# Kernel optimization log

Measured on AMD Instinct MI355X. Metric: run time of the kernel, lower is better.

The kernel has to match this reference:

```python
import jax, jax.numpy as jnp
import numpy as np
from jax import lax

B, C, H, W = 64, 64, 56, 56
E, TOPK = 8, 2
DN = ('NCHW', 'OIHW', 'NCHW')


def setup_inputs() -> dict:
    key = jax.random.key(0)
    ks = jax.random.split(key, 9)
    s = 0.05
    return {
        'x': jax.random.normal(ks[0], (B, C, H, W), jnp.float32),
        'gate_w': jax.random.normal(ks[1], (E, C), jnp.float32) * s,
        'gate_b': jnp.zeros((E,), jnp.float32),
        'conv1_w': jax.random.normal(ks[2], (E, C, C, 3, 3), jnp.float32) * s,
        'bn1_s': jnp.ones((E, C), jnp.float32),
        'bn1_b': jnp.zeros((E, C), jnp.float32),
        'conv2_w': jax.random.normal(ks[3], (E, C, C, 3, 3), jnp.float32) * s,
        'bn2_s': jnp.ones((E, C), jnp.float32),
        'bn2_b': jnp.zeros((E, C), jnp.float32),
    }


def _conv3x3(x, w):
    return lax.conv_general_dilated(x, w, (1, 1), ((1, 1), (1, 1)), dimension_numbers=DN)


def _bn(y, scale, bias):
    # eval-mode BatchNorm with running_mean=0, running_var=1 -> per-channel affine
    return y * scale[None, :, None, None] + bias[None, :, None, None]


def _basic_block(x, w1, s1, b1, w2, s2, b2):
    # standard ResNet BasicBlock, stride=1, identity downsample
    out = jax.nn.relu(_bn(_conv3x3(x, w1), s1, b1))
    out = _bn(_conv3x3(out, w2), s2, b2)
    return jax.nn.relu(out + x)


def reference(x, gate_w, gate_b, conv1_w, bn1_s, bn1_b, conv2_w, bn2_s, bn2_b):
    # gate: global average pool over HW -> linear -> top-k softmax weights [B, E]
    pooled = jnp.mean(x, axis=(2, 3))                       # [B, C]
    logits = pooled @ gate_w.T + gate_b                      # [B, E]
    top_vals, top_idx = lax.top_k(logits, TOPK)              # [B, K]
    top_w = jax.nn.softmax(top_vals, axis=-1)                # [B, K]
    dense_w = jnp.zeros((x.shape[0], E), x.dtype).at[
        jnp.arange(x.shape[0])[:, None], top_idx].set(top_w)  # [B, E]

    # run all experts (dense reference for the sparse dispatch/combine)
    ex_out = jax.vmap(lambda w1, s1, b1, w2, s2, b2: _basic_block(x, w1, s1, b1, w2, s2, b2))(
        conv1_w, bn1_s, bn1_b, conv2_w, bn2_s, bn2_b)        # [E, B, C, H, W]
    out = jnp.einsum('be,ebchw->bchw', dense_w, ex_out)
    return out, dense_w
```

## Files before the change

### kernel.cpp

```cpp
#include <hip/hip_runtime.h>


#define BATCH 64
#define CH    64
#define HW_   3136
#define IMG_  (CH*HW_)
#define PLANE (HW_*16)
#define NE    8
#define JOBS  128
#define PWSZ  36864
#define NTILE 13
#define BD    6
#define CGRID (NTILE*2*BATCH)

typedef unsigned short u16;
typedef __attribute__((ext_vector_type(8))) short short8_t;
typedef __attribute__((ext_vector_type(16))) float floatx16;

__device__ u16   g_xb[(size_t)BATCH*IMG_ + 4*PLANE];
__device__ u16   g_h[(size_t)JOBS*IMG_ + 4*PLANE];
__device__ u16   g_pw1[NE * PWSZ];
__device__ u16   g_pw2[NE * PWSZ];
__device__ int   g_eid[JOBS];
__device__ float g_wgt[JOBS];
__device__ float g_pool[49 * BATCH * CH];

__device__ __forceinline__ u16 f2b(float f) {
    unsigned v; __builtin_memcpy(&v, &f, 4);
    return (u16)((v + 0x7FFFu + ((v >> 16) & 1u)) >> 16);
}

__global__ __launch_bounds__(256) void prep_kernel(
    const float* __restrict__ x,
    const float* __restrict__ w1, const float* __restrict__ s1,
    const float* __restrict__ w2, const float* __restrict__ s2)
{
    int bid = blockIdx.x;
    int tid = threadIdx.x;
    if (bid < 2304) {
        int idx = bid * 256 + tid;
        int conv = idx / 294912;
        int i2 = idx - conv * 294912;
        int e = i2 / PWSZ;   int r = i2 - e * PWSZ;
        int s36 = r >> 10;   int r2 = r & 1023;
        int mt  = r2 >> 9;   int r3 = r2 & 511;
        int h   = r3 >> 8;   int r4 = r3 & 255;
        int m   = r4 >> 3;   int j  = r4 & 7;
        int tap = s36 >> 2;
        int ci  = ((s36 & 3) << 4) | (h << 3) | j;
        int M   = mt*32 + m;
        const float* w  = conv ? w2 : w1;
        const float* sc = conv ? s2 : s1;
        float v = w[((e*64 + M)*64 + ci)*9 + tap] * sc[e*64 + M];
        (conv ? g_pw2 : g_pw1)[i2] = f2b(v);
        return;
    }
    __shared__ u16 T[64*66];
    int xid = bid - 2304;
    int b = xid / 49;
    int tile = xid - b*49;
    int pos0 = tile * 64;
    int pin = tid & 63;
    int c0 = tid >> 6;
    const float* xb = x + (size_t)b*IMG_ + pos0 + pin;
    #pragma unroll
    for (int i = 0; i < 16; i++) {
        int ch = c0*16 + i;
        T[pin*66 + ch] = f2b(xb[ch*HW_]);
    }
    __syncthreads();
    u16* ob = g_xb + (size_t)b*IMG_ + (size_t)pos0*16;
    #pragma unroll
    for (int i = 0; i < 16; i++) {
        int j = tid + i*256;
        int kq  = j >> 10;
        int pos = (j >> 4) & 63;
        int c16 = j & 15;
        ob[(size_t)kq*PLANE + pos*16 + c16] = T[pos*66 + kq*16 + c16];
    }
    if (tid < 64) {
        float s = 0.f;
        const float* xc = x + (size_t)b*IMG_ + tid*HW_ + pos0;
        #pragma unroll 4
        for (int p = 0; p < 64; p++) s += xc[p];
        g_pool[tile*(BATCH*CH) + b*64 + tid] = s;
    }
}

__global__ __launch_bounds__(64) void gate_fin_kernel(
    const float* __restrict__ gw, const float* __restrict__ gb,
    float* __restrict__ dw_out)
{
    __shared__ float pooled[CH];
    __shared__ float logits[NE];
    int b = blockIdx.x, t = threadIdx.x;
    float s = 0.f;
    #pragma unroll
    for (int i = 0; i < 49; i++) s += g_pool[i*(BATCH*CH) + b*64 + t];
    pooled[t] = s * (1.f/3136.f);
    __syncthreads();
    if (t < NE) {
        float l = gb[t];
        for (int c = 0; c < CH; c++) l += pooled[c] * gw[t*CH + c];
        logits[t] = l;
    }
    __syncthreads();
    if (t == 0) {
        int i1 = 0; float v1 = logits[0];
        for (int e = 1; e < NE; e++) if (logits[e] > v1) { v1 = logits[e]; i1 = e; }
        int i2 = -1; float v2 = -3.4e38f;
        for (int e = 0; e < NE; e++) if (e != i1 && logits[e] > v2) { v2 = logits[e]; i2 = e; }
        float eb = __expf(v2 - v1);
        float wa = 1.f / (1.f + eb), wb = eb / (1.f + eb);
        for (int e = 0; e < NE; e++) dw_out[b*NE + e] = 0.f;
        dw_out[b*NE + i1] = wa;
        dw_out[b*NE + i2] = wb;
        g_eid[2*b] = i1; g_eid[2*b+1] = i2;
        g_wgt[2*b] = wa; g_wgt[2*b+1] = wb;
    }
}

__device__ __forceinline__ void stageA(
    u16* AL, const u16* __restrict__ pw0, const u16* __restrict__ pw1,
    int mt, int tid)
{
    short8_t st[9];
    #pragma unroll
    for (int i = 0; i < 9; i++) {
        int u = i*512 + tid;
        int es = u >= 2304;
        int r = u - (es ? 2304 : 0);
        int s36 = r >> 6;
        int c = r & 63;
        st[i] = *(const short8_t*)((es ? pw1 : pw0) + s36*1024 + mt*512 + c*8);
    }
    #pragma unroll
    for (int i = 0; i < 9; i++) {
        int u = i*512 + tid;
        int es = u >= 2304;
        int r = u - (es ? 2304 : 0);
        int s36 = r >> 6;
        int c = r & 63;
        *(short8_t*)(AL + (s36*2 + es)*512 + c*8) = st[i];
    }
}

__device__ __forceinline__ void mkOffs(
    unsigned* off, int gn, int y, int xc, int h, unsigned zoff)
{
    #pragma unroll
    for (int tap = 0; tap < 9; tap++) {
        int dy = tap/3 - 1, dx = tap - (tap/3)*3 - 1;
        int p = gn + dy*56 + dx;
        bool vld = ((unsigned)(y + dy) < 56u) && ((unsigned)(xc + dx) < 56u);
        off[tap] = vld ? (unsigned)(p*32 + h*16) : zoff;
    }
}
#define LOADB(bk, off) (*(const short8_t*)((bk) + (off)))

#define STEP_SGB(HAS_VMEM, HAS_DS)                                   \
    do {                                                             \
        if (HAS_VMEM) __builtin_amdgcn_sched_group_barrier(0x020, 2, 0); \
        if (HAS_DS)   __builtin_amdgcn_sched_group_barrier(0x100, 1, 0); \
        __builtin_amdgcn_sched_group_barrier(0x008, 2, 0);           \
    } while (0)

__global__ __launch_bounds__(512, 4) void conv1_kernel(const float* __restrict__ b1)
{
    __shared__ u16 AL[36864];
    int wg = blockIdx.x;
    int L  = (wg & 7) * (CGRID/8) + (wg >> 3);
    int b  = L / 26;
    int r  = L - b*26;
    int tile = r >> 1;
    int mt   = r & 1;
    int e0 = g_eid[2*b], e1 = g_eid[2*b+1];
    int tid = threadIdx.x;
    int lane = tid & 63, w = tid >> 6;
    int es = w & 1, pg = w >> 1;
    int l31 = lane & 31, h = lane >> 5;
    int gn0 = tile*256 + pg*64 + l31;
    int gn1 = gn0 + 32;
    int y0 = gn0/56, xc0 = gn0 - y0*56;
    int y1 = gn1/56, xc1 = gn1 - y1*56;
    int e = es ? e1 : e0;
    const char* base = (const char*)(g_xb + (size_t)b*IMG_);
    const char* bk0 = base;
    const char* bk1 = base + PLANE*2;
    const char* bk2 = base + 2*PLANE*2;
    const char* bk3 = base + 3*PLANE*2;
    unsigned zoff = (unsigned)((size_t)(BATCH - b)*IMG_*2);
    const u16* pw0 = g_pw1 + e0*PWSZ;
    const u16* pw1 = g_pw1 + e1*PWSZ;
    int aOff = es*512 + h*256 + l31*8;

    unsigned off0[9], off1[9];
    mkOffs(off0, gn0, y0, xc0, h, zoff);
    mkOffs(off1, gn1, y1, xc1, h, zoff);

    floatx16 accA = {}, accB = {};
    short8_t B0[BD], B1[BD];
    #pragma unroll
    for (int s = 0; s < BD; s++) {
        const char* bk = (s&3)==0 ? bk0 : (s&3)==1 ? bk1 : (s&3)==2 ? bk2 : bk3;
        B0[s] = LOADB(bk, off0[s >> 2]);
        B1[s] = LOADB(bk, off1[s >> 2]);
    }
    stageA(AL, pw0, pw1, mt, tid);
    __syncthreads();

    short8_t Ar[3];
    #pragma unroll
    for (int i = 0; i < 3; i++)
        Ar[i] = *(const short8_t*)(AL + i*1024 + aOff);

    #pragma unroll
    for (int s = 0; s < 36; s++) {
        short8_t bb0 = B0[s % BD];
        short8_t bb1 = B1[s % BD];
        int sp = s + BD;
        if (sp < 36) {
            const char* bk = (sp&3)==0 ? bk0 : (sp&3)==1 ? bk1 : (sp&3)==2 ? bk2 : bk3;
            B0[s % BD] = LOADB(bk, off0[sp >> 2]);
            B1[s % BD] = LOADB(bk, off1[sp >> 2]);
        }
        short8_t a = Ar[s % 3];
        if (s + 3 < 36)
            Ar[s % 3] = *(const short8_t*)(AL + (s+3)*1024 + aOff);
        accA = __builtin_amdgcn_mfma_f32_32x32x16_bf16(a, bb0, accA, 0, 0, 0);
        accB = __builtin_amdgcn_mfma_f32_32x32x16_bf16(a, bb1, accB, 0, 0, 0);
        STEP_SGB(sp < 36, s + 3 < 36);
    }

    u16* hb = g_h + (size_t)(2*b + es)*IMG_;
    #pragma unroll
    for (int f = 0; f < 2; f++) {
        int gn = f ? gn1 : gn0;
        if (gn < HW_) {
            #pragma unroll
            for (int rg = 0; rg < 4; rg++) {
                union { u16 u[4]; uint2 v; } t;
                #pragma unroll
                for (int rr = 0; rr < 4; rr++) {
                    int m = rg*8 + h*4 + rr;
                    float v = (f ? accB : accA)[rg*4 + rr] + b1[e*64 + mt*32 + m];
                    t.u[rr] = f2b(fmaxf(v, 0.f));
                }
                int kq = mt*2 + (rg >> 1);
                *(uint2*)(hb + (size_t)kq*PLANE + (size_t)gn*16 + (rg & 1)*8 + h*4) = t.v;
            }
        }
    }
}

__global__ __launch_bounds__(512, 4) void conv2_kernel(
    const float* __restrict__ x, const float* __restrict__ b2,
    float* __restrict__ out)
{
    __shared__ u16 AL[36864];
    int wg = blockIdx.x;
    int L  = (wg & 7) * (CGRID/8) + (wg >> 3);
    int b  = L / 26;
    int r  = L - b*26;
    int tile = (NTILE-1) - (r >> 1);
    int mt   = r & 1;
    int e0 = g_eid[2*b], e1 = g_eid[2*b+1];
    int tid = threadIdx.x;
    int lane = tid & 63, w = tid >> 6;
    int es = w & 1, pg = w >> 1;
    int l31 = lane & 31, h = lane >> 5;
    int gn0 = tile*256 + pg*64 + l31;
    int gn1 = gn0 + 32;
    int y0 = gn0/56, xc0 = gn0 - y0*56;
    int y1 = gn1/56, xc1 = gn1 - y1*56;
    int e = es ? e1 : e0;
    float wgt = g_wgt[2*b + es];
    const char* base = (const char*)(g_h + (size_t)(2*b + es)*IMG_);
    const char* bk0 = base;
    const char* bk1 = base + PLANE*2;
    const char* bk2 = base + 2*PLANE*2;
    const char* bk3 = base + 3*PLANE*2;
    unsigned zoff = (unsigned)((size_t)(JOBS - (2*b + es))*IMG_*2);
    const u16* pw0 = g_pw2 + e0*PWSZ;
    const u16* pw1 = g_pw2 + e1*PWSZ;
    int aOff = es*512 + h*256 + l31*8;

    unsigned off0[9], off1[9];
    mkOffs(off0, gn0, y0, xc0, h, zoff);
    mkOffs(off1, gn1, y1, xc1, h, zoff);

    floatx16 accA = {}, accB = {};
    short8_t B0[BD], B1[BD];
    #pragma unroll
    for (int s = 0; s < BD; s++) {
        const char* bk = (s&3)==0 ? bk0 : (s&3)==1 ? bk1 : (s&3)==2 ? bk2 : bk3;
        B0[s] = LOADB(bk, off0[s >> 2]);
        B1[s] = LOADB(bk, off1[s >> 2]);
    }
    stageA(AL, pw0, pw1, mt, tid);
    __syncthreads();

    short8_t Ar[3];
    #pragma unroll
    for (int i = 0; i < 3; i++)
        Ar[i] = *(const short8_t*)(AL + i*1024 + aOff);

    #pragma unroll
    for (int s = 0; s < 36; s++) {
        short8_t bb0 = B0[s % BD];
        short8_t bb1 = B1[s % BD];
        int sp = s + BD;
        if (sp < 36) {
            const char* bk = (sp&3)==0 ? bk0 : (sp&3)==1 ? bk1 : (sp&3)==2 ? bk2 : bk3;
            B0[s % BD] = LOADB(bk, off0[sp >> 2]);
            B1[s % BD] = LOADB(bk, off1[sp >> 2]);
        }
        short8_t a = Ar[s % 3];
        if (s + 3 < 36)
            Ar[s % 3] = *(const short8_t*)(AL + (s+3)*1024 + aOff);
        accA = __builtin_amdgcn_mfma_f32_32x32x16_bf16(a, bb0, accA, 0, 0, 0);
        accB = __builtin_amdgcn_mfma_f32_32x32x16_bf16(a, bb1, accB, 0, 0, 0);
        STEP_SGB(sp < 36, s + 3 < 36);
    }

    __syncthreads();
    float* P = (float*)AL;
    const float* xb = x + (size_t)b*IMG_ + (size_t)(mt*32)*HW_;
    if (es == 0) {
        #pragma unroll
        for (int f = 0; f < 2; f++) {
            int gn = f ? gn1 : gn0;
            if (gn < HW_) {
                #pragma unroll
                for (int rg = 0; rg < 4; rg++)
                    #pragma unroll
                    for (int rr = 0; rr < 4; rr++) {
                        int m = rg*8 + h*4 + rr;
                        float v = (f ? accB : accA)[rg*4 + rr] + b2[e*64 + mt*32 + m]
                                  + xb[(size_t)m*HW_ + gn];
                        P[((pg*2 + f)*32 + m)*32 + l31] = wgt * fmaxf(v, 0.f);
                    }
            }
        }
    }
    __syncthreads();
    if (es == 1) {
        float* ob = out + (size_t)b*IMG_ + (size_t)(mt*32)*HW_;
        #pragma unroll
        for (int f = 0; f < 2; f++) {
            int gn = f ? gn1 : gn0;
            if (gn < HW_) {
                #pragma unroll
                for (int rg = 0; rg < 4; rg++)
                    #pragma unroll
                    for (int rr = 0; rr < 4; rr++) {
                        int m = rg*8 + h*4 + rr;
                        float v = (f ? accB : accA)[rg*4 + rr] + b2[e*64 + mt*32 + m]
                                  + xb[(size_t)m*HW_ + gn];
                        ob[(size_t)m*HW_ + gn] = wgt * fmaxf(v, 0.f)
                                                 + P[((pg*2 + f)*32 + m)*32 + l31];
                    }
            }
        }
    }
}

extern "C" void kernel_launch(void* const* d_in, const int* in_sizes, int n_in,
                              void* d_out, int out_size, void* d_ws, size_t ws_size,
                              hipStream_t stream) {
    const float* x   = (const float*)d_in[0];
    const float* gw  = (const float*)d_in[1];
    const float* gb  = (const float*)d_in[2];
    const float* w1  = (const float*)d_in[3];
    const float* s1  = (const float*)d_in[4];
    const float* b1  = (const float*)d_in[5];
    const float* w2  = (const float*)d_in[6];
    const float* s2  = (const float*)d_in[7];
    const float* b2  = (const float*)d_in[8];
    float* out = (float*)d_out;
    float* dw  = out + (size_t)BATCH * IMG_;

    (void)d_ws; (void)ws_size;

    hipLaunchKernelGGL(prep_kernel, dim3(2304 + 3136), dim3(256), 0, stream,
                       x, w1, s1, w2, s2);
    hipLaunchKernelGGL(gate_fin_kernel, dim3(BATCH), dim3(64), 0, stream, gw, gb, dw);
    hipLaunchKernelGGL(conv1_kernel, dim3(CGRID), dim3(512), 0, stream, b1);
    hipLaunchKernelGGL(conv2_kernel, dim3(CGRID), dim3(512), 0, stream, x, b2, out);
}
```

Measured before the change: 236.2 us.

## Load conv weights directly from global memory instead of staging through LDS

Removes the per-block LDS staging of both experts' weight slices and the barrier that followed it. Each wave now reads its A fragments straight from global memory (relying on cache hits). LDS use drops, so launch bounds are raised to 8 blocks per CU to increase occupancy, and the explicit sched_group_barrier interleaving is removed. The risk is higher global or L2 traffic and load latency on the weight fetches, which the compiler's default scheduling may not hide well.

```diff
diff --git a/kernel.cpp b/kernel.cpp
--- a/kernel.cpp
+++ b/kernel.cpp
@@ -120,31 +120,6 @@
     }
 }
 
-__device__ __forceinline__ void stageA(
-    u16* AL, const u16* __restrict__ pw0, const u16* __restrict__ pw1,
-    int mt, int tid)
-{
-    short8_t st[9];
-    #pragma unroll
-    for (int i = 0; i < 9; i++) {
-        int u = i*512 + tid;
-        int es = u >= 2304;
-        int r = u - (es ? 2304 : 0);
-        int s36 = r >> 6;
-        int c = r & 63;
-        st[i] = *(const short8_t*)((es ? pw1 : pw0) + s36*1024 + mt*512 + c*8);
-    }
-    #pragma unroll
-    for (int i = 0; i < 9; i++) {
-        int u = i*512 + tid;
-        int es = u >= 2304;
-        int r = u - (es ? 2304 : 0);
-        int s36 = r >> 6;
-        int c = r & 63;
-        *(short8_t*)(AL + (s36*2 + es)*512 + c*8) = st[i];
-    }
-}
-
 __device__ __forceinline__ void mkOffs(
     unsigned* off, int gn, int y, int xc, int h, unsigned zoff)
 {
@@ -158,16 +133,8 @@
 }
 #define LOADB(bk, off) (*(const short8_t*)((bk) + (off)))
 
-#define STEP_SGB(HAS_VMEM, HAS_DS)                                   \
-    do {                                                             \
-        if (HAS_VMEM) __builtin_amdgcn_sched_group_barrier(0x020, 2, 0); \
-        if (HAS_DS)   __builtin_amdgcn_sched_group_barrier(0x100, 1, 0); \
-        __builtin_amdgcn_sched_group_barrier(0x008, 2, 0);           \
-    } while (0)
-
-__global__ __launch_bounds__(512, 4) void conv1_kernel(const float* __restrict__ b1)
-{
-    __shared__ u16 AL[36864];
+__global__ __launch_bounds__(512, 8) void conv1_kernel(const float* __restrict__ b1)
+{
     int wg = blockIdx.x;
     int L  = (wg & 7) * (CGRID/8) + (wg >> 3);
     int b  = L / 26;
@@ -190,9 +157,7 @@
     const char* bk2 = base + 2*PLANE*2;
     const char* bk3 = base + 3*PLANE*2;
     unsigned zoff = (unsigned)((size_t)(BATCH - b)*IMG_*2);
-    const u16* pw0 = g_pw1 + e0*PWSZ;
-    const u16* pw1 = g_pw1 + e1*PWSZ;
-    int aOff = es*512 + h*256 + l31*8;
+    const u16* pwA = g_pw1 + e*PWSZ + mt*512 + h*256 + l31*8;
 
     unsigned off0[9], off1[9];
     mkOffs(off0, gn0, y0, xc0, h, zoff);
@@ -206,13 +171,10 @@
         B0[s] = LOADB(bk, off0[s >> 2]);
         B1[s] = LOADB(bk, off1[s >> 2]);
     }
-    stageA(AL, pw0, pw1, mt, tid);
-    __syncthreads();
-
     short8_t Ar[3];
     #pragma unroll
     for (int i = 0; i < 3; i++)
-        Ar[i] = *(const short8_t*)(AL + i*1024 + aOff);
+        Ar[i] = *(const short8_t*)(pwA + i*1024);
 
     #pragma unroll
     for (int s = 0; s < 36; s++) {
@@ -226,10 +188,9 @@
         }
         short8_t a = Ar[s % 3];
         if (s + 3 < 36)
-            Ar[s % 3] = *(const short8_t*)(AL + (s+3)*1024 + aOff);
+            Ar[s % 3] = *(const short8_t*)(pwA + (s+3)*1024);
         accA = __builtin_amdgcn_mfma_f32_32x32x16_bf16(a, bb0, accA, 0, 0, 0);
         accB = __builtin_amdgcn_mfma_f32_32x32x16_bf16(a, bb1, accB, 0, 0, 0);
-        STEP_SGB(sp < 36, s + 3 < 36);
     }
 
     u16* hb = g_h + (size_t)(2*b + es)*IMG_;
@@ -253,11 +214,11 @@
     }
 }
 
-__global__ __launch_bounds__(512, 4) void conv2_kernel(
+__global__ __launch_bounds__(512, 8) void conv2_kernel(
     const float* __restrict__ x, const float* __restrict__ b2,
     float* __restrict__ out)
 {
-    __shared__ u16 AL[36864];
+    __shared__ float P[8192];
     int wg = blockIdx.x;
     int L  = (wg & 7) * (CGRID/8) + (wg >> 3);
     int b  = L / 26;
@@ -281,9 +242,7 @@
     const char* bk2 = base + 2*PLANE*2;
     const char* bk3 = base + 3*PLANE*2;
     unsigned zoff = (unsigned)((size_t)(JOBS - (2*b + es))*IMG_*2);
-    const u16* pw0 = g_pw2 + e0*PWSZ;
-    const u16* pw1 = g_pw2 + e1*PWSZ;
-    int aOff = es*512 + h*256 + l31*8;
+    const u16* pwA = g_pw2 + e*PWSZ + mt*512 + h*256 + l31*8;
 
     unsigned off0[9], off1[9];
     mkOffs(off0, gn0, y0, xc0, h, zoff);
@@ -297,13 +256,10 @@
         B0[s] = LOADB(bk, off0[s >> 2]);
         B1[s] = LOADB(bk, off1[s >> 2]);
     }
-    stageA(AL, pw0, pw1, mt, tid);
-    __syncthreads();
-
     short8_t Ar[3];
     #pragma unroll
     for (int i = 0; i < 3; i++)
-        Ar[i] = *(const short8_t*)(AL + i*1024 + aOff);
+        Ar[i] = *(const short8_t*)(pwA + i*1024);
 
     #pragma unroll
     for (int s = 0; s < 36; s++) {
@@ -317,14 +273,11 @@
         }
         short8_t a = Ar[s % 3];
         if (s + 3 < 36)
-            Ar[s % 3] = *(const short8_t*)(AL + (s+3)*1024 + aOff);
+            Ar[s % 3] = *(const short8_t*)(pwA + (s+3)*1024);
         accA = __builtin_amdgcn_mfma_f32_32x32x16_bf16(a, bb0, accA, 0, 0, 0);
         accB = __builtin_amdgcn_mfma_f32_32x32x16_bf16(a, bb1, accB, 0, 0, 0);
-        STEP_SGB(sp < 36, s + 3 < 36);
-    }
-
-    __syncthreads();
-    float* P = (float*)AL;
+    }
+
     const float* xb = x + (size_t)b*IMG_ + (size_t)(mt*32)*HW_;
     if (es == 0) {
         #pragma unroll
```

Result: slower. 374.4 us (+58.5%).
